# Performance work log

Measured on AMD Instinct MI355X. Metric: run time of the kernel, lower is better.

Reference implementation:

```python
import jax, jax.numpy as jnp
import numpy as np

NUM_HEADS = 16
NUM_KV_HEADS = 4
HEAD_DIM = 128
ROPE_BASE = 10000.0


def _apply_rope(x):
    # x: [B, H, S, D], interleaved RoPE: x1 = x[..., ::2], x2 = x[..., 1::2]
    B, H, S, D = x.shape
    inv_freq = 1.0 / (ROPE_BASE ** (jnp.arange(0, D, 2, dtype=jnp.float32) / D))  # [D/2]
    t = jnp.arange(S, dtype=jnp.float32)
    freqs = t[:, None] * inv_freq[None, :]          # [S, D/2]
    cos = jnp.cos(freqs)[None, None]                # [1,1,S,D/2]
    sin = jnp.sin(freqs)[None, None]
    xr = x.reshape(B, H, S, D // 2, 2)
    x1, x2 = xr[..., 0], xr[..., 1]
    r1 = x1 * cos - x2 * sin
    r2 = x1 * sin + x2 * cos
    return jnp.stack([r1, r2], axis=-1).reshape(B, H, S, D)


def setup_inputs() -> dict:
    key = jax.random.key(0)
    ks = jax.random.split(key, 5)
    H = NUM_HEADS * HEAD_DIM          # 2048
    KV = NUM_KV_HEADS * HEAD_DIM      # 512
    std = 0.02
    return {
        "hidden_states": jax.random.normal(ks[0], (1, 4096, H), dtype=jnp.float32),
        "wq": jax.random.normal(ks[1], (H, H), dtype=jnp.float32) * std,
        "wk": jax.random.normal(ks[2], (H, KV), dtype=jnp.float32) * std,
        "wv": jax.random.normal(ks[3], (H, KV), dtype=jnp.float32) * std,
        "wo": jax.random.normal(ks[4], (H, H), dtype=jnp.float32) * std,
    }


def reference(hidden_states, wq, wk, wv, wo):
    B, S, H = hidden_states.shape
    nh, nkv, hd = NUM_HEADS, NUM_KV_HEADS, HEAD_DIM
    scale = 1.0 / np.sqrt(hd)

    q = (hidden_states @ wq).reshape(B, S, nh, hd).transpose(0, 2, 1, 3)   # [B,nh,S,hd]
    k = (hidden_states @ wk).reshape(B, S, nkv, hd).transpose(0, 2, 1, 3)  # [B,nkv,S,hd]
    v = (hidden_states @ wv).reshape(B, S, nkv, hd).transpose(0, 2, 1, 3)

    q = _apply_rope(q)
    k = _apply_rope(k)

    rep = nh // nkv
    k = jnp.repeat(k, rep, axis=1)  # GQA head repetition -> [B,nh,S,hd]
    v = jnp.repeat(v, rep, axis=1)

    scores = jnp.einsum("bhqd,bhkd->bhqk", q, k) * scale
    causal = jnp.tril(jnp.ones((S, S), dtype=bool))
    scores = jnp.where(causal[None, None], scores, jnp.float32(-1e30))
    probs = jax.nn.softmax(scores, axis=-1)
    attn = jnp.einsum("bhqk,bhkd->bhqd", probs, v)      # [B,nh,S,hd]
    attn = attn.transpose(0, 2, 1, 3).reshape(B, S, H)
    return attn @ wo
```

## Files before the change

### kernel.cpp

```cpp
#include <hip/hip_runtime.h>

typedef unsigned short u16;
typedef unsigned int u32;
typedef __bf16 bf16x8 __attribute__((ext_vector_type(8)));
typedef float f32x4 __attribute__((ext_vector_type(4)));
typedef float f32x16 __attribute__((ext_vector_type(16)));
typedef int v2i __attribute__((ext_vector_type(2)));

#define S_LEN 4096
#define HDIM 2048
#define KVDIM 512
#define N_HEADS 16
#define HEAD_D 128

__device__ __forceinline__ u16 f2bf(float f) {
  u32 u = __float_as_uint(f);
  u32 r = (u + 0x7FFFu + ((u >> 16) & 1u)) >> 16;
  return (u16)r;
}
__device__ __forceinline__ float bf2f(u16 h) {
  return __uint_as_float(((u32)h) << 16);
}
__device__ __forceinline__ float exp2_fast(float x) {
  float r;
  asm("v_exp_f32 %0, %1" : "=v"(r) : "v"(x));
  return r;
}
__device__ __forceinline__ u32 cvt_pk_bf16(float lo, float hi) {
  u32 r;
  asm("v_cvt_pk_bf16_f32 %0, %1, %2" : "=v"(r) : "v"(lo), "v"(hi));
  return r;
}
__device__ __forceinline__ void gload16(const u16* g, u16* l) {
  __builtin_amdgcn_global_load_lds(
      (const __attribute__((address_space(1))) void*)g,
      (__attribute__((address_space(3))) void*)l, 16, 0, 0);
}

__global__ void k_cast_bf16(const float* __restrict__ in, u16* __restrict__ out, int n8) {
  int i = blockIdx.x * blockDim.x + threadIdx.x;
  if (i >= n8) return;
  const float4* p = reinterpret_cast<const float4*>(in) + (size_t)i * 2;
  float4 a = p[0], b = p[1];
  u32 o0 = (u32)f2bf(a.x) | ((u32)f2bf(a.y) << 16);
  u32 o1 = (u32)f2bf(a.z) | ((u32)f2bf(a.w) << 16);
  u32 o2 = (u32)f2bf(b.x) | ((u32)f2bf(b.y) << 16);
  u32 o3 = (u32)f2bf(b.z) | ((u32)f2bf(b.w) << 16);
  reinterpret_cast<uint4*>(out)[i] = make_uint4(o0, o1, o2, o3);
}

__global__ void k_transpose_cast(const float* __restrict__ W, u16* __restrict__ Wt,
                                 int Kd, int Nd) {
  __shared__ float t[32][33];
  int bx = blockIdx.x, by = blockIdx.y;
  int tx = threadIdx.x, ty = threadIdx.y;
  int n = bx * 32 + tx;
  for (int j = ty; j < 32; j += 8)
    t[j][tx] = W[(size_t)(by * 32 + j) * Nd + n];
  __syncthreads();
  int k = by * 32 + tx;
  for (int j = ty; j < 32; j += 8)
    Wt[(size_t)(bx * 32 + j) * Kd + k] = f2bf(t[tx][j]);
}

__global__ void k_rope_table(float* __restrict__ cosT, float* __restrict__ sinT) {
  int i = blockIdx.x * blockDim.x + threadIdx.x;
  int pos = i >> 6, f = i & 63;
  float inv = expf(-0.1439115683121279f * (float)f);
  float ang = (float)pos * inv;
  float s, c;
  sincosf(ang, &s, &c);
  cosT[i] = c;
  sinT[i] = s;
}

__global__ void k_rope_apply(u16* __restrict__ X, const float* __restrict__ cosT,
                             const float* __restrict__ sinT, int width) {
  int i = blockIdx.x * blockDim.x + threadIdx.x;
  size_t idx = (size_t)i * 8;
  int row = (int)(idx / width);
  int col = (int)(idx - (size_t)row * width);
  int fi = (col & 127) >> 1;
  float4 c4 = *reinterpret_cast<const float4*>(&cosT[(row << 6) + fi]);
  float4 s4 = *reinterpret_cast<const float4*>(&sinT[(row << 6) + fi]);
  uint4 v = *reinterpret_cast<const uint4*>(&X[idx]);
  float cc[4] = {c4.x, c4.y, c4.z, c4.w};
  float ss[4] = {s4.x, s4.y, s4.z, s4.w};
  u32 w_[4] = {v.x, v.y, v.z, v.w};
  u32 r_[4];
#pragma unroll
  for (int p = 0; p < 4; ++p) {
    float x1 = bf2f((u16)(w_[p] & 0xffff));
    float x2 = bf2f((u16)(w_[p] >> 16));
    float r1 = x1 * cc[p] - x2 * ss[p];
    float r2 = x1 * ss[p] + x2 * cc[p];
    r_[p] = (u32)f2bf(r1) | ((u32)f2bf(r2) << 16);
  }
  *reinterpret_cast<uint4*>(&X[idx]) = make_uint4(r_[0], r_[1], r_[2], r_[3]);
}

__global__ __launch_bounds__(256) void k_gemm_qkv(
    const u16* __restrict__ A, const u16* __restrict__ WqT, const u16* __restrict__ WkT,
    const u16* __restrict__ WvT, u16* __restrict__ Qb, u16* __restrict__ Kb,
    u16* __restrict__ VTb) {
  const int Kd = HDIM, M = S_LEN;
  __shared__ __align__(16) u16 As[128 * 32];
  __shared__ __align__(16) u16 Bs[128 * 32];
  const int by = blockIdx.y;
  const u16* Bt;
  int bn, N, mode;
  if (by < 16) { Bt = WqT; bn = by * 128; N = HDIM; mode = 0; }
  else if (by < 20) { Bt = WkT; bn = (by - 16) * 128; N = KVDIM; mode = 1; }
  else { Bt = WvT; bn = (by - 20) * 128; N = KVDIM; mode = 2; }
  const int bm = blockIdx.x * 128;
  const int tid = threadIdx.x;
  const int lane = tid & 63;
  const int wid = tid >> 6;
  const int wr = (wid >> 1) * 64, wc = (wid & 1) * 64;
  const int lr = lane & 15, lhi = lane >> 4;
  const int srow = lane >> 2;
  const int skc = (lane & 3) * 8;
  f32x4 acc[4][4] = {};
  for (int k0 = 0; k0 < Kd; k0 += 32) {
#pragma unroll
    for (int it = 0; it < 2; ++it) {
      int rowbase = (it * 4 + wid) * 16;
      gload16(&A[(size_t)(bm + rowbase + srow) * Kd + k0 + skc], &As[rowbase * 32]);
      gload16(&Bt[(size_t)(bn + rowbase + srow) * Kd + k0 + skc], &Bs[rowbase * 32]);
    }
    __syncthreads();
    bf16x8 af[4], bfr[4];
#pragma unroll
    for (int m = 0; m < 4; ++m)
      af[m] = *reinterpret_cast<const bf16x8*>(&As[(wr + m * 16 + lr) * 32 + lhi * 8]);
#pragma unroll
    for (int n = 0; n < 4; ++n)
      bfr[n] = *reinterpret_cast<const bf16x8*>(&Bs[(wc + n * 16 + lr) * 32 + lhi * 8]);
#pragma unroll
    for (int m = 0; m < 4; ++m)
#pragma unroll
      for (int n = 0; n < 4; ++n)
        acc[m][n] = __builtin_amdgcn_mfma_f32_16x16x32_bf16(af[m], bfr[n], acc[m][n], 0, 0, 0);
    __syncthreads();
  }
#pragma unroll
  for (int m = 0; m < 4; ++m) {
    int grow0 = bm + wr + m * 16 + lhi * 4;
#pragma unroll
    for (int n = 0; n < 4; ++n) {
      int gcol = bn + wc + n * 16 + lr;
      if (mode == 2) {
        ushort4 pk;
        pk.x = f2bf(acc[m][n][0]);
        pk.y = f2bf(acc[m][n][1]);
        pk.z = f2bf(acc[m][n][2]);
        pk.w = f2bf(acc[m][n][3]);
        *reinterpret_cast<ushort4*>(&VTb[(size_t)gcol * M + grow0]) = pk;
      } else {
        u16* outp = (mode == 0) ? Qb : Kb;
#pragma unroll
        for (int r = 0; r < 4; ++r)
          outp[(size_t)(grow0 + r) * N + gcol] = f2bf(acc[m][n][r]);
      }
    }
  }
}

__global__ __launch_bounds__(256) void k_gemm_bt(
    const u16* __restrict__ A, const u16* __restrict__ Bt, float* __restrict__ Cout,
    int M, int N, int Kd) {
  __shared__ __align__(16) u16 As[128 * 32];
  __shared__ __align__(16) u16 Bs[128 * 32];
  const int bm = blockIdx.x * 128;
  const int bn = blockIdx.y * 128;
  const int tid = threadIdx.x;
  const int lane = tid & 63;
  const int wid = tid >> 6;
  const int wr = (wid >> 1) * 64, wc = (wid & 1) * 64;
  const int lr = lane & 15, lhi = lane >> 4;
  const int srow = lane >> 2;
  const int skc = (lane & 3) * 8;
  f32x4 acc[4][4] = {};
  for (int k0 = 0; k0 < Kd; k0 += 32) {
#pragma unroll
    for (int it = 0; it < 2; ++it) {
      int rowbase = (it * 4 + wid) * 16;
      gload16(&A[(size_t)(bm + rowbase + srow) * Kd + k0 + skc], &As[rowbase * 32]);
      gload16(&Bt[(size_t)(bn + rowbase + srow) * Kd + k0 + skc], &Bs[rowbase * 32]);
    }
    __syncthreads();
    bf16x8 af[4], bfr[4];
#pragma unroll
    for (int m = 0; m < 4; ++m)
      af[m] = *reinterpret_cast<const bf16x8*>(&As[(wr + m * 16 + lr) * 32 + lhi * 8]);
#pragma unroll
    for (int n = 0; n < 4; ++n)
      bfr[n] = *reinterpret_cast<const bf16x8*>(&Bs[(wc + n * 16 + lr) * 32 + lhi * 8]);
#pragma unroll
    for (int m = 0; m < 4; ++m)
#pragma unroll
      for (int n = 0; n < 4; ++n)
        acc[m][n] = __builtin_amdgcn_mfma_f32_16x16x32_bf16(af[m], bfr[n], acc[m][n], 0, 0, 0);
    __syncthreads();
  }
#pragma unroll
  for (int m = 0; m < 4; ++m) {
    int grow0 = bm + wr + m * 16 + lhi * 4;
#pragma unroll
    for (int n = 0; n < 4; ++n) {
      int gcol = bn + wc + n * 16 + lr;
#pragma unroll
      for (int r = 0; r < 4; ++r)
        Cout[(size_t)(grow0 + r) * N + gcol] = acc[m][n][r];
    }
  }
}

__global__ __launch_bounds__(256, 2) void k_attn(
    const u16* __restrict__ Q, const u16* __restrict__ K, const u16* __restrict__ VT,
    u16* __restrict__ O) {
  __shared__ __align__(16) u16 Ks[64 * 128];
  __shared__ __align__(16) u16 Vs[128 * 64];
  int i = blockIdx.x;
  int qt, h;
  if (i < 256) { qt = 16 + (i & 15); h = i >> 4; }
  else { int jj = i - 256; qt = 15 - (jj & 15); h = jj >> 4; }
  const int kvh = h >> 2;
  const int tid = threadIdx.x, lane = tid & 63, wid = tid >> 6;
  const int l31 = lane & 31, hi = lane >> 5;
  const int qw = qt * 128 + wid * 32;
  const int qglob = qw + l31;
  const float CE = 0.12751743f;
  const float THR = 62.74f;

  const u16* qptr = &Q[(size_t)qglob * HDIM + h * HEAD_D];
  bf16x8 qf[8];
#pragma unroll
  for (int ks = 0; ks < 8; ++ks)
    qf[ks] = *reinterpret_cast<const bf16x8*>(&qptr[ks * 16 + hi * 8]);

  f32x16 o_[4] = {};
  float m_ = -3e38f, l_ = 0.f;
  char* KsB = (char*)Ks;
  char* VsB = (char*)Vs;

  const int nst = 2 * qt + 2;
  for (int j = 0; j < nst; ++j) {
    const int kb = j << 6;
    __syncthreads();
#pragma unroll
    for (int it = 0; it < 4; ++it) {
      int s = it * 256 + tid;
      int kv = s >> 4, c16 = s & 15;
      int db = kv * 256 + c16 * 16;
      db ^= ((db >> 8) & 7) << 4;
      *reinterpret_cast<uint4*>(KsB + db) = *reinterpret_cast<const uint4*>(
          &K[(size_t)(kb + kv) * KVDIM + kvh * HEAD_D + c16 * 8]);
    }
#pragma unroll
    for (int it = 0; it < 4; ++it) {
      int s = it * 256 + tid;
      int d = s >> 3, k16 = s & 7;
      int db = d * 128 + k16 * 16;
      db ^= ((db >> 7) & 7) << 4;
      *reinterpret_cast<uint4*>(VsB + db) = *reinterpret_cast<const uint4*>(
          &VT[(size_t)(kvh * HEAD_D + d) * S_LEN + kb + k16 * 8]);
    }
    __syncthreads();

    if (kb <= qw + 31) {
      f32x16 s0 = {}, s1 = {};
#pragma unroll
      for (int ks = 0; ks < 8; ++ks) {
        int db0 = l31 * 256 + ks * 32 + hi * 16;
        db0 ^= ((db0 >> 8) & 7) << 4;
        int db1 = (32 + l31) * 256 + ks * 32 + hi * 16;
        db1 ^= ((db1 >> 8) & 7) << 4;
        bf16x8 k0 = *reinterpret_cast<const bf16x8*>(KsB + db0);
        bf16x8 k1 = *reinterpret_cast<const bf16x8*>(KsB + db1);
        s0 = __builtin_amdgcn_mfma_f32_32x32x16_bf16(k0, qf[ks], s0, 0, 0, 0);
        s1 = __builtin_amdgcn_mfma_f32_32x32x16_bf16(k1, qf[ks], s1, 0, 0, 0);
      }
      if (kb + 63 > qw) {
#pragma unroll
        for (int r = 0; r < 16; ++r) {
          int kvr = kb + (r & 3) + 8 * (r >> 2) + 4 * hi;
          if (kvr > qglob) s0[r] = -1e30f;
          if (kvr + 32 > qglob) s1[r] = -1e30f;
        }
      }
      float pm = fmaxf(s0[0], s1[0]);
#pragma unroll
      for (int r = 1; r < 16; ++r) pm = fmaxf(pm, fmaxf(s0[r], s1[r]));
      pm = fmaxf(pm, __shfl_xor(pm, 32));
      if (!__all(pm <= m_ + THR)) {
        float mnew = fmaxf(m_, pm);
        float fac = exp2_fast((m_ - mnew) * CE);
        m_ = mnew;
        l_ *= fac;
#pragma unroll
        for (int dt = 0; dt < 4; ++dt)
#pragma unroll
          for (int r = 0; r < 16; ++r) o_[dt][r] *= fac;
      }
      const float mc = m_ * CE;
      float rs = 0.f;
#pragma unroll
      for (int r = 0; r < 16; ++r) {
        s0[r] = exp2_fast(__builtin_fmaf(s0[r], CE, -mc));
        s1[r] = exp2_fast(__builtin_fmaf(s1[r], CE, -mc));
        rs += s0[r] + s1[r];
      }
      rs += __shfl_xor(rs, 32);
      l_ += rs;
#pragma unroll
      for (int kvt = 0; kvt < 2; ++kvt) {
        u32 xw[8], yw[8];
#pragma unroll
        for (int g = 0; g < 8; ++g) {
          float plo = kvt ? s1[2 * g] : s0[2 * g];
          float phi = kvt ? s1[2 * g + 1] : s0[2 * g + 1];
          u32 pw = cvt_pk_bf16(plo, phi);
          v2i sw = __builtin_amdgcn_permlane32_swap((int)pw, (int)pw, false, false);
          xw[g] = (u32)sw[0];
          yw[g] = (u32)sw[1];
        }
#pragma unroll
        for (int ksl = 0; ksl < 2; ++ksl) {
          int b = ksl * 4;
          u32 f0 = hi ? xw[b + 2] : xw[b + 0];
          u32 f1 = hi ? xw[b + 3] : xw[b + 1];
          u32 f2 = hi ? yw[b + 2] : yw[b + 0];
          u32 f3 = hi ? yw[b + 3] : yw[b + 1];
          uint4 fr = make_uint4(f0, f1, f2, f3);
          bf16x8 pf = *reinterpret_cast<bf16x8*>(&fr);
          const int kvstep = kvt * 2 + ksl;
#pragma unroll
          for (int dt = 0; dt < 4; ++dt) {
            int db = (dt * 32 + l31) * 128 + kvstep * 32 + hi * 16;
            db ^= ((db >> 7) & 7) << 4;
            bf16x8 vf = *reinterpret_cast<const bf16x8*>(VsB + db);
            o_[dt] = __builtin_amdgcn_mfma_f32_32x32x16_bf16(vf, pf, o_[dt], 0, 0, 0);
          }
        }
      }
    }
  }
  const float inv_l = 1.0f / l_;
  u16* optr = &O[(size_t)qglob * HDIM + h * HEAD_D];
#pragma unroll
  for (int dt = 0; dt < 4; ++dt)
#pragma unroll
    for (int g = 0; g < 4; ++g) {
      ushort4 pk;
      pk.x = f2bf(o_[dt][4 * g + 0] * inv_l);
      pk.y = f2bf(o_[dt][4 * g + 1] * inv_l);
      pk.z = f2bf(o_[dt][4 * g + 2] * inv_l);
      pk.w = f2bf(o_[dt][4 * g + 3] * inv_l);
      *reinterpret_cast<ushort4*>(&optr[dt * 32 + g * 8 + hi * 4]) = pk;
    }
}

extern "C" void kernel_launch(void* const* d_in, const int* in_sizes, int n_in,
                              void* d_out, int out_size, void* d_ws, size_t ws_size,
                              hipStream_t stream) {
  const float* hs = (const float*)d_in[0];
  const float* wq = (const float*)d_in[1];
  const float* wk = (const float*)d_in[2];
  const float* wv = (const float*)d_in[3];
  const float* wo = (const float*)d_in[4];

  char* ws = (char*)d_ws;
  size_t off = 0;
  auto alloc = [&](size_t bytes) {
    void* p = ws + off;
    off += (bytes + 255) & ~(size_t)255;
    return p;
  };
  u16* Xb = (u16*)alloc((size_t)S_LEN * HDIM * 2);
  u16* WqT = (u16*)alloc((size_t)HDIM * HDIM * 2);
  u16* WkT = (u16*)alloc((size_t)KVDIM * HDIM * 2);
  u16* WvT = (u16*)alloc((size_t)KVDIM * HDIM * 2);
  u16* WoT = (u16*)alloc((size_t)HDIM * HDIM * 2);
  u16* Qb = (u16*)alloc((size_t)S_LEN * HDIM * 2);
  u16* Kb = (u16*)alloc((size_t)S_LEN * KVDIM * 2);
  u16* VTb = (u16*)alloc((size_t)KVDIM * S_LEN * 2);
  u16* Ab = (u16*)alloc((size_t)S_LEN * HDIM * 2);
  float* cosT = (float*)alloc((size_t)S_LEN * 64 * 4);
  float* sinT = (float*)alloc((size_t)S_LEN * 64 * 4);
  if (off > ws_size) return;

  k_cast_bf16<<<dim3(S_LEN * HDIM / 8 / 256), dim3(256), 0, stream>>>(hs, Xb, S_LEN * HDIM / 8);
  k_transpose_cast<<<dim3(HDIM / 32, HDIM / 32), dim3(32, 8), 0, stream>>>(wq, WqT, HDIM, HDIM);
  k_transpose_cast<<<dim3(KVDIM / 32, HDIM / 32), dim3(32, 8), 0, stream>>>(wk, WkT, HDIM, KVDIM);
  k_transpose_cast<<<dim3(KVDIM / 32, HDIM / 32), dim3(32, 8), 0, stream>>>(wv, WvT, HDIM, KVDIM);
  k_transpose_cast<<<dim3(HDIM / 32, HDIM / 32), dim3(32, 8), 0, stream>>>(wo, WoT, HDIM, HDIM);
  k_rope_table<<<dim3(S_LEN * 64 / 256), dim3(256), 0, stream>>>(cosT, sinT);
  k_gemm_qkv<<<dim3(32, 24), dim3(256), 0, stream>>>(Xb, WqT, WkT, WvT, Qb, Kb, VTb);
  k_rope_apply<<<dim3(S_LEN * HDIM / 8 / 256), dim3(256), 0, stream>>>(Qb, cosT, sinT, HDIM);
  k_rope_apply<<<dim3(S_LEN * KVDIM / 8 / 256), dim3(256), 0, stream>>>(Kb, cosT, sinT, KVDIM);
  k_attn<<<dim3(512), dim3(256), 0, stream>>>(Qb, Kb, VTb, Ab);
  k_gemm_bt<<<dim3(32, 16), dim3(256), 0, stream>>>(Ab, WoT, (float*)d_out, S_LEN, HDIM, HDIM);
}
```

Before: 294.6 us.

## Double-buffer attention K/V tiles with async global-to-LDS loads

The attention kernel now keeps two LDS buffers for K and V. It prefetches the next 64-key tile with global_load_lds while the current tile is being computed on. The XOR swizzle moves from the LDS destination to the global source addresses, so the direct-to-LDS loads keep the same layout. One barrier per iteration is removed. In exchange, LDS use per block doubles, and correctness relies on the remaining barrier waiting for the outstanding async loads.

```diff
diff --git a/kernel.cpp b/kernel.cpp
--- a/kernel.cpp
+++ b/kernel.cpp
@@ -31,7 +31,7 @@
   asm("v_cvt_pk_bf16_f32 %0, %1, %2" : "=v"(r) : "v"(lo), "v"(hi));
   return r;
 }
-__device__ __forceinline__ void gload16(const u16* g, u16* l) {
+__device__ __forceinline__ void gload16(const u16* g, const u16* l) {
   __builtin_amdgcn_global_load_lds(
       (const __attribute__((address_space(1))) void*)g,
       (__attribute__((address_space(3))) void*)l, 16, 0, 0);
@@ -219,8 +219,8 @@
 __global__ __launch_bounds__(256, 2) void k_attn(
     const u16* __restrict__ Q, const u16* __restrict__ K, const u16* __restrict__ VT,
     u16* __restrict__ O) {
-  __shared__ __align__(16) u16 Ks[64 * 128];
-  __shared__ __align__(16) u16 Vs[128 * 64];
+  __shared__ __align__(16) u16 Ks[2][64 * 128];
+  __shared__ __align__(16) u16 Vs[2][128 * 64];
   int i = blockIdx.x;
   int qt, h;
   if (i < 256) { qt = 16 + (i & 15); h = i >> 4; }
@@ -241,32 +241,34 @@
 
   f32x16 o_[4] = {};
   float m_ = -3e38f, l_ = 0.f;
-  char* KsB = (char*)Ks;
-  char* VsB = (char*)Vs;
+
+  const int skv = (wid * 64 + lane) >> 4;
+  const int sc16 = ((wid * 64 + lane) & 15) ^ (skv & 7);
+  const int sd = (wid * 64 + lane) >> 3;
+  const int sk16 = ((wid * 64 + lane) & 7) ^ (sd & 7);
+  const int sbase = wid * 64;
+
+  auto stage = [&](int buf, int kb) {
+#pragma unroll
+    for (int it = 0; it < 4; ++it) {
+      gload16(&K[(size_t)(kb + it * 16 + skv) * KVDIM + kvh * HEAD_D + sc16 * 8],
+              (const u16*)((const char*)&Ks[buf][0] + (it * 256 + sbase) * 16));
+    }
+#pragma unroll
+    for (int it = 0; it < 4; ++it) {
+      gload16(&VT[(size_t)(kvh * HEAD_D + it * 32 + sd) * S_LEN + kb + sk16 * 8],
+              (const u16*)((const char*)&Vs[buf][0] + (it * 256 + sbase) * 16));
+    }
+  };
 
   const int nst = 2 * qt + 2;
+  stage(0, 0);
   for (int j = 0; j < nst; ++j) {
     const int kb = j << 6;
     __syncthreads();
-#pragma unroll
-    for (int it = 0; it < 4; ++it) {
-      int s = it * 256 + tid;
-      int kv = s >> 4, c16 = s & 15;
-      int db = kv * 256 + c16 * 16;
-      db ^= ((db >> 8) & 7) << 4;
-      *reinterpret_cast<uint4*>(KsB + db) = *reinterpret_cast<const uint4*>(
-          &K[(size_t)(kb + kv) * KVDIM + kvh * HEAD_D + c16 * 8]);
-    }
-#pragma unroll
-    for (int it = 0; it < 4; ++it) {
-      int s = it * 256 + tid;
-      int d = s >> 3, k16 = s & 7;
-      int db = d * 128 + k16 * 16;
-      db ^= ((db >> 7) & 7) << 4;
-      *reinterpret_cast<uint4*>(VsB + db) = *reinterpret_cast<const uint4*>(
-          &VT[(size_t)(kvh * HEAD_D + d) * S_LEN + kb + k16 * 8]);
-    }
-    __syncthreads();
+    if (j + 1 < nst) stage((j + 1) & 1, (j + 1) << 6);
+    const char* KsB = (const char*)&Ks[j & 1][0];
+    const char* VsB = (const char*)&Vs[j & 1][0];
 
     if (kb <= qw + 31) {
       f32x16 s0 = {}, s1 = {};
```

Result: slower. 340.1 us (+15.4%).

## Prefetch next K/V tile into registers during attention compute

Applied to the files above, without the earlier changes.

The flash-attention loop now issues the global loads for the next 64-key K and V^T tile into registers right after the current tile is stored to LDS. Those loads overlap with the QK MFMA and softmax work, hiding global memory latency. Address and swizzle offsets are also precomputed once outside the loop. The cost is 32 extra VGPRs for the staging registers, which may reduce occupancy.

```diff
diff --git a/kernel.cpp b/kernel.cpp
--- a/kernel.cpp
+++ b/kernel.cpp
@@ -31,7 +31,7 @@
   asm("v_cvt_pk_bf16_f32 %0, %1, %2" : "=v"(r) : "v"(lo), "v"(hi));
   return r;
 }
-__device__ __forceinline__ void gload16(const u16* g, u16* l) {
+__device__ __forceinline__ void gload16(const u16* g, const u16* l) {
   __builtin_amdgcn_global_load_lds(
       (const __attribute__((address_space(1))) void*)g,
       (__attribute__((address_space(3))) void*)l, 16, 0, 0);
@@ -244,29 +244,51 @@
   char* KsB = (char*)Ks;
   char* VsB = (char*)Vs;
 
+  const u16* kbase[4];
+  const u16* vbase[4];
+  int kdb[4], vdb[4];
+#pragma unroll
+  for (int it = 0; it < 4; ++it) {
+    int kv = it * 16 + (tid >> 4), c16 = tid & 15;
+    kbase[it] = K + (size_t)kv * KVDIM + kvh * HEAD_D + c16 * 8;
+    int db = kv * 256 + c16 * 16;
+    db ^= ((db >> 8) & 7) << 4;
+    kdb[it] = db;
+    int d = it * 32 + (tid >> 3), k16 = tid & 7;
+    vbase[it] = VT + (size_t)(kvh * HEAD_D + d) * S_LEN + k16 * 8;
+    int db2 = d * 128 + k16 * 16;
+    db2 ^= ((db2 >> 7) & 7) << 4;
+    vdb[it] = db2;
+  }
+  uint4 kreg[4], vreg[4];
+
   const int nst = 2 * qt + 2;
+#pragma unroll
+  for (int it = 0; it < 4; ++it)
+    kreg[it] = *reinterpret_cast<const uint4*>(kbase[it]);
+#pragma unroll
+  for (int it = 0; it < 4; ++it)
+    vreg[it] = *reinterpret_cast<const uint4*>(vbase[it]);
+
   for (int j = 0; j < nst; ++j) {
     const int kb = j << 6;
     __syncthreads();
 #pragma unroll
-    for (int it = 0; it < 4; ++it) {
-      int s = it * 256 + tid;
-      int kv = s >> 4, c16 = s & 15;
-      int db = kv * 256 + c16 * 16;
-      db ^= ((db >> 8) & 7) << 4;
-      *reinterpret_cast<uint4*>(KsB + db) = *reinterpret_cast<const uint4*>(
-          &K[(size_t)(kb + kv) * KVDIM + kvh * HEAD_D + c16 * 8]);
-    }
-#pragma unroll
-    for (int it = 0; it < 4; ++it) {
-      int s = it * 256 + tid;
-      int d = s >> 3, k16 = s & 7;
-      int db = d * 128 + k16 * 16;
-      db ^= ((db >> 7) & 7) << 4;
-      *reinterpret_cast<uint4*>(VsB + db) = *reinterpret_cast<const uint4*>(
-          &VT[(size_t)(kvh * HEAD_D + d) * S_LEN + kb + k16 * 8]);
-    }
-    __syncthreads();
+    for (int it = 0; it < 4; ++it)
+      *reinterpret_cast<uint4*>(KsB + kdb[it]) = kreg[it];
+#pragma unroll
+    for (int it = 0; it < 4; ++it)
+      *reinterpret_cast<uint4*>(VsB + vdb[it]) = vreg[it];
+    __syncthreads();
+    if (j + 1 < nst) {
+      const int kb1 = (j + 1) << 6;
+#pragma unroll
+      for (int it = 0; it < 4; ++it)
+        kreg[it] = *reinterpret_cast<const uint4*>(kbase[it] + (size_t)kb1 * KVDIM);
+#pragma unroll
+      for (int it = 0; it < 4; ++it)
+        vreg[it] = *reinterpret_cast<const uint4*>(vbase[it] + kb1);
+    }
 
     if (kb <= qw + 31) {
       f32x16 s0 = {}, s1 = {};
```

Measured after the change: 387.5 us. 1.32x slower.
